# Kernel optimization log

Hardware: AMD Instinct MI355X
Metric: run time of the kernel (lower is better)

## Reference

```python
import jax, jax.numpy as jnp
import numpy as np

B, T, D, H = 16, 1024, 2048, 512


def _lstm_dir(x, w_ih, w_hh, b_ih, b_hh, reverse):
    # x: (B,T,Din); w_ih: (4H,Din); w_hh: (4H,H). PyTorch gate order: i,f,g,o.
    h_dim = w_hh.shape[1]
    xg = jnp.einsum('btd,gd->btg', x, w_ih) + b_ih + b_hh  # (B,T,4H) input gates precomputed

    def step(carry, xg_t):
        h, c = carry
        g = xg_t + h @ w_hh.T
        i, f, gg, o = jnp.split(g, 4, axis=-1)
        i = jax.nn.sigmoid(i)
        f = jax.nn.sigmoid(f)
        gg = jnp.tanh(gg)
        o = jax.nn.sigmoid(o)
        c = f * c + i * gg
        h = o * jnp.tanh(c)
        return (h, c), h

    b = x.shape[0]
    init = (jnp.zeros((b, h_dim), x.dtype), jnp.zeros((b, h_dim), x.dtype))
    _, hs = jax.lax.scan(step, init, jnp.swapaxes(xg, 0, 1), reverse=reverse)
    return jnp.swapaxes(hs, 0, 1)  # (B,T,H)


def _bilstm_layer(x, p_fwd, p_bwd):
    out_f = _lstm_dir(x, *p_fwd, reverse=False)
    out_b = _lstm_dir(x, *p_bwd, reverse=True)
    return jnp.concatenate([out_f, out_b], axis=-1)  # (B,T,2H)


def setup_inputs() -> dict:
    key = jax.random.key(0)
    ks = jax.random.split(key, 20)
    s = 1.0 / np.sqrt(H)

    def u(k, shape):
        return jax.random.uniform(k, shape, jnp.float32, -s, s)

    inp = {'x': jax.random.normal(ks[0], (B, T, D), jnp.float32)}
    i = 1
    for layer, din in [(0, D), (1, 2 * H)]:
        for suf in ['', '_rev']:
            inp[f'w_ih_l{layer}{suf}'] = u(ks[i], (4 * H, din)); i += 1
            inp[f'w_hh_l{layer}{suf}'] = u(ks[i], (4 * H, H)); i += 1
            inp[f'b_ih_l{layer}{suf}'] = u(ks[i], (4 * H,)); i += 1
            inp[f'b_hh_l{layer}{suf}'] = u(ks[i], (4 * H,)); i += 1
            i -= 2  # reuse keys sparingly
            inp[f'b_ih_l{layer}{suf}'] = u(jax.random.fold_in(ks[i], 1), (4 * H,))
            inp[f'b_hh_l{layer}{suf}'] = u(jax.random.fold_in(ks[i], 2), (4 * H,))
            i += 2
    inp['attn_w'] = u(ks[17], (1, 2 * H))
    inp['attn_b'] = u(ks[18], (1,))
    return inp


def reference(x,
              w_ih_l0, w_hh_l0, b_ih_l0, b_hh_l0,
              w_ih_l0_rev, w_hh_l0_rev, b_ih_l0_rev, b_hh_l0_rev,
              w_ih_l1, w_hh_l1, b_ih_l1, b_hh_l1,
              w_ih_l1_rev, w_hh_l1_rev, b_ih_l1_rev, b_hh_l1_rev,
              attn_w, attn_b):
    out = _bilstm_layer(x,
                        (w_ih_l0, w_hh_l0, b_ih_l0, b_hh_l0),
                        (w_ih_l0_rev, w_hh_l0_rev, b_ih_l0_rev, b_hh_l0_rev))
    out = _bilstm_layer(out,
                        (w_ih_l1, w_hh_l1, b_ih_l1, b_hh_l1),
                        (w_ih_l1_rev, w_hh_l1_rev, b_ih_l1_rev, b_hh_l1_rev))
    # attention pooling: Linear(2H -> 1), softmax over time, weighted sum
    scores = jnp.einsum('bth,oh->bto', out, attn_w) + attn_b  # (B,T,1)
    weights = jax.nn.softmax(scores, axis=1)
    encoding = jnp.sum(weights * out, axis=1)  # (B, 2H)
    return encoding
```

## Files before the change

kernel.cpp:

```cpp
#include <hip/hip_runtime.h>
#include <hip/hip_bf16.h>
#include <cstdio>

typedef unsigned short ushort_t;
typedef unsigned long long u64;
typedef __attribute__((ext_vector_type(4))) float f32x4;
typedef __attribute__((ext_vector_type(4))) unsigned int u32x4;
typedef __attribute__((ext_vector_type(8))) __bf16 bf16x8;
typedef __attribute__((ext_vector_type(8))) unsigned short u16x8;
typedef __attribute__((ext_vector_type(4))) unsigned short u16x4;

#define B_  16
#define T_  1024
#define H_  512
#define NG  2048
#define M_  (B_*T_)
#define NBLK_DIR 16
#define FLG_STRIDE 64

__device__ inline unsigned short f2bf_rne(float f){
  union { float f; unsigned int u; } v; v.f = f;
  unsigned int u = v.u;
  unsigned int r = (u + 0x7fffu + ((u >> 16) & 1u)) >> 16;
  return (unsigned short)r;
}
__device__ inline float bf2f(unsigned short s){
  union { unsigned int u; float f; } v; v.u = ((unsigned int)s) << 16;
  return v.f;
}
__device__ inline float sigm_f(float x){
  return 1.0f / (1.0f + __expf(-x));
}
__device__ inline float tanh_f(float x){
  return 1.0f - 2.0f / (__expf(2.0f * x) + 1.0f);
}

__global__ void zero_u32(unsigned* __restrict__ p, int n){
  int i = blockIdx.x * blockDim.x + threadIdx.x;
  if (i < n) p[i] = 0u;
}

__global__ void split_f32_bf16(const float* __restrict__ src,
                               ushort_t* __restrict__ hi, ushort_t* __restrict__ lo,
                               int n4){
  int i = blockIdx.x * blockDim.x + threadIdx.x;
  int stride = gridDim.x * blockDim.x;
  for (; i < n4; i += stride){
    f32x4 v = ((const f32x4*)src)[i];
    u16x4 h4, l4;
    #pragma unroll
    for (int j = 0; j < 4; j++){
      unsigned short h = f2bf_rne(v[j]);
      h4[j] = h;
      l4[j] = f2bf_rne(v[j] - bf2f(h));
    }
    ((u16x4*)hi)[i] = h4;
    ((u16x4*)lo)[i] = l4;
  }
}

__global__ __launch_bounds__(256) void gemm_xg(
    const ushort_t* __restrict__ Ahi, const ushort_t* __restrict__ Alo,
    const ushort_t* __restrict__ Bhi0, const ushort_t* __restrict__ Blo0,
    const ushort_t* __restrict__ Bhi1, const ushort_t* __restrict__ Blo1,
    const float* __restrict__ bi0, const float* __restrict__ bh0,
    const float* __restrict__ bi1, const float* __restrict__ bh1,
    float* __restrict__ C0, float* __restrict__ C1,
    int M, int N, int K)
{
  __shared__ ushort_t As[128*32];
  __shared__ ushort_t Bs[128*32];
  const int tid  = threadIdx.x;
  const int wave = tid >> 6, lane = tid & 63;
  const int l15 = lane & 15, l4 = lane >> 4;
  const int wr = wave >> 1, wc = wave & 1;
  const int n0 = blockIdx.x * 128, m0 = blockIdx.y * 128;
  const int dir = blockIdx.z;
  const ushort_t* Bhi = dir ? Bhi1 : Bhi0;
  const ushort_t* Blo = dir ? Blo1 : Blo0;
  const float* bia = dir ? bi1 : bi0;
  const float* bib = dir ? bh1 : bh0;
  float* C = dir ? C1 : C0;

  f32x4 acc[4][4];
  #pragma unroll
  for (int i = 0; i < 4; i++)
    #pragma unroll
    for (int j = 0; j < 4; j++) acc[i][j] = (f32x4){0.f,0.f,0.f,0.f};

  const int e0 = tid, e1 = 256 + tid;
  const int row0 = e0 >> 2, c80 = (e0 & 3) * 8;
  const int row1 = e1 >> 2, c81 = (e1 & 3) * 8;

  for (int seg = 0; seg < 3; ++seg){
    const ushort_t* Ap = (seg == 2) ? Alo : Ahi;
    const ushort_t* Bp = (seg == 1) ? Blo : Bhi;
    for (int kt = 0; kt < K; kt += 32){
      __builtin_amdgcn_global_load_lds(
        (const __attribute__((address_space(1))) unsigned int*)(Ap + (size_t)(m0 + row0) * K + kt + c80),
        (__attribute__((address_space(3))) unsigned int*)(As + e0 * 8), 16, 0, 0);
      __builtin_amdgcn_global_load_lds(
        (const __attribute__((address_space(1))) unsigned int*)(Bp + (size_t)(n0 + row0) * K + kt + c80),
        (__attribute__((address_space(3))) unsigned int*)(Bs + e0 * 8), 16, 0, 0);
      __builtin_amdgcn_global_load_lds(
        (const __attribute__((address_space(1))) unsigned int*)(Ap + (size_t)(m0 + row1) * K + kt + c81),
        (__attribute__((address_space(3))) unsigned int*)(As + e1 * 8), 16, 0, 0);
      __builtin_amdgcn_global_load_lds(
        (const __attribute__((address_space(1))) unsigned int*)(Bp + (size_t)(n0 + row1) * K + kt + c81),
        (__attribute__((address_space(3))) unsigned int*)(Bs + e1 * 8), 16, 0, 0);
      __syncthreads();
      bf16x8 af[4], bfr[4];
      #pragma unroll
      for (int m = 0; m < 4; m++)
        af[m] = *(const bf16x8*)(As + (wr*64 + m*16 + l15) * 32 + l4 * 8);
      #pragma unroll
      for (int n = 0; n < 4; n++)
        bfr[n] = *(const bf16x8*)(Bs + (wc*64 + n*16 + l15) * 32 + l4 * 8);
      #pragma unroll
      for (int m = 0; m < 4; m++)
        #pragma unroll
        for (int n = 0; n < 4; n++)
          acc[m][n] = __builtin_amdgcn_mfma_f32_16x16x32_bf16(af[m], bfr[n], acc[m][n], 0, 0, 0);
      __syncthreads();
    }
  }
  #pragma unroll
  for (int m = 0; m < 4; m++)
    #pragma unroll
    for (int n = 0; n < 4; n++){
      int col = n0 + wc*64 + n*16 + l15;
      float bias = bia[col] + bib[col];
      #pragma unroll
      for (int r = 0; r < 4; r++){
        int row = m0 + wr*64 + m*16 + l4*4 + r;
        C[(size_t)row * N + col] = acc[m][n][r] + bias;
      }
    }
}

__global__ __launch_bounds__(512, 1) void lstm_layer(
    const float* __restrict__ whh_fwd, const float* __restrict__ whh_bwd,
    const float* __restrict__ xg,
    u64* __restrict__ hbuf,
    unsigned* __restrict__ flags,
    float* __restrict__ out_f32,
    ushort_t* __restrict__ out_hi,
    ushort_t* __restrict__ out_lo)
{
  const int dir = blockIdx.x >> 4;
  const int cb  = blockIdx.x & 15;
  const int tid = threadIdx.x;
  const int wave = tid >> 6, lane = tid & 63;
  const int gate = wave >> 1, ch = wave & 1;
  const int l15 = lane & 15, l4 = lane >> 4;
  const float* whh = dir ? whh_bwd : whh_fwd;
  u64* hb = hbuf + (size_t)dir * 2 * 8192;
  unsigned* flg = flags + (size_t)dir * FLG_STRIDE;

  __shared__ ushort_t hfhi[8192];
  __shared__ ushort_t hflo[8192];
  __shared__ float gbuf[4][16][33];

  bf16x8 Whi[16], Wlo[16];
  {
    const int wrow = gate * 512 + cb * 32 + ch * 16 + l15;
    const float* p0 = whh + (size_t)wrow * 512;
    #pragma unroll
    for (int s = 0; s < 16; s++){
      const float* p = p0 + s * 32 + l4 * 8;
      f32x4 va = *(const f32x4*)(p);
      f32x4 vb = *(const f32x4*)(p + 4);
      u16x8 th, tl;
      #pragma unroll
      for (int j = 0; j < 4; j++){
        unsigned short h = f2bf_rne(va[j]);
        th[j] = h; tl[j] = f2bf_rne(va[j] - bf2f(h));
        unsigned short h2 = f2bf_rne(vb[j]);
        th[4+j] = h2; tl[4+j] = f2bf_rne(vb[j] - bf2f(h2));
      }
      Whi[s] = __builtin_bit_cast(bf16x8, th);
      Wlo[s] = __builtin_bit_cast(bf16x8, tl);
    }
  }

  const int eb = tid >> 5, ecl = tid & 31, ecol = cb * 32 + ecl;

  const int srow = (tid >> 2) & 15;
  const int tq = tid >> 6;
  const int sbase = srow * 512 + (tq >> 2) * 32 + (tq & 3) * 8 + (tid & 3) * 2;

  __hip_atomic_store(&hb[eb * 512 + ecol], (u64)1u << 32, __ATOMIC_RELAXED, __HIP_MEMORY_SCOPE_AGENT);
  if (tid == 0)
    __hip_atomic_store(&flg[cb], 1u, __ATOMIC_RELAXED, __HIP_MEMORY_SCOPE_AGENT);

  float c_state = 0.0f;

  for (int t = 0; t < T_; ++t){
    const int t_eff = dir ? (T_ - 1 - t) : t;
    const float* xgp = xg + ((size_t)dir * M_ + (size_t)eb * T_ + t_eff) * NG + ecol;
    float xi = xgp[0];
    float xf = xgp[512];
    float xgg = xgp[1024];
    float xo = xgp[1536];

    const unsigned want = (unsigned)(t + 1);
    if (tid < NBLK_DIR){
      while (__hip_atomic_load(&flg[tid], __ATOMIC_RELAXED, __HIP_MEMORY_SCOPE_AGENT) < want)
        __builtin_amdgcn_s_sleep(1);
    }
    __syncthreads();

    const u64* src = hb + (size_t)(t & 1) * 8192;
    u64 va[8], vb[8];
    #pragma unroll
    for (int i = 0; i < 8; i++){
      va[i] = __hip_atomic_load(&src[sbase + i * 64],     __ATOMIC_RELAXED, __HIP_MEMORY_SCOPE_AGENT);
      vb[i] = __hip_atomic_load(&src[sbase + i * 64 + 1], __ATOMIC_RELAXED, __HIP_MEMORY_SCOPE_AGENT);
    }
    for (;;){
      unsigned stale = 0;
      #pragma unroll
      for (int i = 0; i < 8; i++){
        if ((unsigned)(va[i] >> 32) != want || (unsigned)(vb[i] >> 32) != want)
          stale |= 1u << i;
      }
      if (!stale) break;
      #pragma unroll
      for (int i = 0; i < 8; i++){
        if (stale & (1u << i)){
          va[i] = __hip_atomic_load(&src[sbase + i * 64],     __ATOMIC_RELAXED, __HIP_MEMORY_SCOPE_AGENT);
          vb[i] = __hip_atomic_load(&src[sbase + i * 64 + 1], __ATOMIC_RELAXED, __HIP_MEMORY_SCOPE_AGENT);
        }
      }
    }
    #pragma unroll
    for (int i = 0; i < 8; i++){
      unsigned d0 = (unsigned)va[i], d1 = (unsigned)vb[i];
      ((unsigned*)hfhi)[i * 512 + tid] = (d0 & 0xffffu) | (d1 << 16);
      ((unsigned*)hflo)[i * 512 + tid] = (d0 >> 16) | (d1 & 0xffff0000u);
    }
    __syncthreads();

    {
      f32x4 a0 = {0.f,0.f,0.f,0.f}, a1 = a0, a2 = a0;
      #pragma unroll
      for (int s = 0; s < 16; s++){
        bf16x8 ah = *(const bf16x8*)&hfhi[(s * 64 + l4 * 16 + l15) * 8];
        bf16x8 al = *(const bf16x8*)&hflo[(s * 64 + l4 * 16 + l15) * 8];
        a0 = __builtin_amdgcn_mfma_f32_16x16x32_bf16(ah, Whi[s], a0, 0, 0, 0);
        a1 = __builtin_amdgcn_mfma_f32_16x16x32_bf16(ah, Wlo[s], a1, 0, 0, 0);
        a2 = __builtin_amdgcn_mfma_f32_16x16x32_bf16(al, Whi[s], a2, 0, 0, 0);
      }
      f32x4 acc = a0 + a1;
      acc = acc + a2;
      #pragma unroll
      for (int r = 0; r < 4; r++)
        gbuf[gate][l4 * 4 + r][ch * 16 + l15] = acc[r];
    }
    __syncthreads();

    {
      float pi = gbuf[0][eb][ecl] + xi;
      float pf = gbuf[1][eb][ecl] + xf;
      float pg = gbuf[2][eb][ecl] + xgg;
      float po = gbuf[3][eb][ecl] + xo;
      float ig = sigm_f(pi);
      float fg = sigm_f(pf);
      float gg = tanh_f(pg);
      float og = sigm_f(po);
      c_state = fg * c_state + ig * gg;
      float h = og * tanh_f(c_state);
      unsigned short hh = f2bf_rne(h);
      unsigned short hl = f2bf_rne(h - bf2f(hh));
      unsigned pack = (unsigned)hh | ((unsigned)hl << 16);
      u64 v = ((u64)(unsigned)(t + 2) << 32) | (u64)pack;
      __hip_atomic_store(&hb[(size_t)((t + 1) & 1) * 8192 + eb * 512 + ecol], v,
                         __ATOMIC_RELAXED, __HIP_MEMORY_SCOPE_AGENT);
      if (tid == 0)
        __hip_atomic_store(&flg[cb], (unsigned)(t + 2), __ATOMIC_RELAXED, __HIP_MEMORY_SCOPE_AGENT);
      size_t oidx = ((size_t)eb * T_ + t_eff) * 1024 + dir * 512 + ecol;
      if (out_f32) out_f32[oidx] = h;
      if (out_hi){ out_hi[oidx] = hh; out_lo[oidx] = hl; }
    }
  }
}

__device__ inline float dot4(f32x4 a, f32x4 b){
  return a[0]*b[0] + a[1]*b[1] + a[2]*b[2] + a[3]*b[3];
}

__global__ __launch_bounds__(256) void attn_pool(
    const float* __restrict__ out1,
    const float* __restrict__ aw,
    const float* __restrict__ ab,
    float* __restrict__ enc)
{
  __shared__ float wbuf[1024];
  __shared__ float sc[1024];
  __shared__ float red[16];
  const int b = blockIdx.x;
  const int tid = threadIdx.x;
  const int wave = tid >> 6, lane = tid & 63;
  ((f32x4*)wbuf)[tid] = ((const f32x4*)aw)[tid];
  __syncthreads();
  const float* ob = out1 + (size_t)b * T_ * 1024;
  const float bias = ab[0];

  for (int t = wave; t < T_; t += 4){
    const float* row = ob + (size_t)t * 1024;
    float s = dot4(((const f32x4*)row)[lane],       ((const f32x4*)wbuf)[lane])
            + dot4(((const f32x4*)row)[lane + 64],  ((const f32x4*)wbuf)[lane + 64])
            + dot4(((const f32x4*)row)[lane + 128], ((const f32x4*)wbuf)[lane + 128])
            + dot4(((const f32x4*)row)[lane + 192], ((const f32x4*)wbuf)[lane + 192]);
    #pragma unroll
    for (int o = 32; o > 0; o >>= 1) s += __shfl_xor(s, o, 64);
    if (lane == 0) sc[t] = s + bias;
  }
  __syncthreads();

  float m = -1e30f;
  for (int i = tid; i < 1024; i += 256) m = fmaxf(m, sc[i]);
  #pragma unroll
  for (int o = 32; o > 0; o >>= 1) m = fmaxf(m, __shfl_xor(m, o, 64));
  if (lane == 0) red[wave] = m;
  __syncthreads();
  m = fmaxf(fmaxf(red[0], red[1]), fmaxf(red[2], red[3]));

  float ssum = 0.f;
  for (int i = tid; i < 1024; i += 256){
    float p = __expf(sc[i] - m);
    sc[i] = p;
    ssum += p;
  }
  #pragma unroll
  for (int o = 32; o > 0; o >>= 1) ssum += __shfl_xor(ssum, o, 64);
  if (lane == 0) red[8 + wave] = ssum;
  __syncthreads();
  float inv = 1.0f / (red[8] + red[9] + red[10] + red[11]);

  f32x4 a = {0.f,0.f,0.f,0.f};
  for (int t = 0; t < T_; t++){
    f32x4 v = *(const f32x4*)(ob + (size_t)t * 1024 + tid * 4);
    float p = sc[t];
    a[0] += p * v[0]; a[1] += p * v[1]; a[2] += p * v[2]; a[3] += p * v[3];
  }
  f32x4 r = { a[0]*inv, a[1]*inv, a[2]*inv, a[3]*inv };
  *(f32x4*)(enc + (size_t)b * 1024 + tid * 4) = r;
}

extern "C" void kernel_launch(void* const* d_in, const int* in_sizes, int n_in,
                              void* d_out, int out_size, void* d_ws, size_t ws_size,
                              hipStream_t stream)
{
  const float* x        = (const float*)d_in[0];
  const float* w_ih_l0  = (const float*)d_in[1];
  const float* w_hh_l0  = (const float*)d_in[2];
  const float* b_ih_l0  = (const float*)d_in[3];
  const float* b_hh_l0  = (const float*)d_in[4];
  const float* w_ih_l0r = (const float*)d_in[5];
  const float* w_hh_l0r = (const float*)d_in[6];
  const float* b_ih_l0r = (const float*)d_in[7];
  const float* b_hh_l0r = (const float*)d_in[8];
  const float* w_ih_l1  = (const float*)d_in[9];
  const float* w_hh_l1  = (const float*)d_in[10];
  const float* b_ih_l1  = (const float*)d_in[11];
  const float* b_hh_l1  = (const float*)d_in[12];
  const float* w_ih_l1r = (const float*)d_in[13];
  const float* w_hh_l1r = (const float*)d_in[14];
  const float* b_ih_l1r = (const float*)d_in[15];
  const float* b_hh_l1r = (const float*)d_in[16];
  const float* attn_w   = (const float*)d_in[17];
  const float* attn_b   = (const float*)d_in[18];
  float* enc = (float*)d_out;

  char* ws = (char*)d_ws;
  size_t off = 0;
  auto alloc = [&](size_t bytes) -> void* {
    void* p = ws + off;
    off += (bytes + 255) & ~(size_t)255;
    return p;
  };
  ushort_t* Ahi  = (ushort_t*)alloc((size_t)M_ * 2048 * 2);
  ushort_t* Alo  = (ushort_t*)alloc((size_t)M_ * 2048 * 2);
  ushort_t* Whi0 = (ushort_t*)alloc((size_t)2048 * 2048 * 2);
  ushort_t* Wlo0 = (ushort_t*)alloc((size_t)2048 * 2048 * 2);
  ushort_t* Whi1 = (ushort_t*)alloc((size_t)2048 * 2048 * 2);
  ushort_t* Wlo1 = (ushort_t*)alloc((size_t)2048 * 2048 * 2);
  float*    xg   = (float*)alloc((size_t)2 * M_ * NG * 4);
  float*    outb = (float*)alloc((size_t)M_ * 1024 * 4);
  u64*      hbuf = (u64*)alloc((size_t)2 * 2 * 2 * 8192 * 8);
  unsigned* flags= (unsigned*)alloc((size_t)2 * 2 * FLG_STRIDE * 4);
  if (off > ws_size){
    fprintf(stderr, "kernel_launch: workspace too small: need %zu have %zu\n", off, ws_size);
    return;
  }

  {
    int n = (int)((size_t)2 * 2 * 2 * 8192 * 8 / 4) + 2 * 2 * FLG_STRIDE;
    zero_u32<<<(n + 255) / 256, 256, 0, stream>>>((unsigned*)hbuf, n);
  }

  split_f32_bf16<<<2048, 256, 0, stream>>>(x, Ahi, Alo, M_ * 2048 / 4);
  split_f32_bf16<<<512, 256, 0, stream>>>(w_ih_l0,  Whi0, Wlo0, 2048 * 2048 / 4);
  split_f32_bf16<<<512, 256, 0, stream>>>(w_ih_l0r, Whi1, Wlo1, 2048 * 2048 / 4);
  gemm_xg<<<dim3(16, 128, 2), 256, 0, stream>>>(
      Ahi, Alo, Whi0, Wlo0, Whi1, Wlo1,
      b_ih_l0, b_hh_l0, b_ih_l0r, b_hh_l0r,
      xg, xg + (size_t)M_ * NG, M_, NG, 2048);
  lstm_layer<<<32, 512, 0, stream>>>(w_hh_l0, w_hh_l0r, xg, hbuf, flags,
                                     nullptr, Ahi, Alo);
  split_f32_bf16<<<512, 256, 0, stream>>>(w_ih_l1,  Whi0, Wlo0, 2048 * 1024 / 4);
  split_f32_bf16<<<512, 256, 0, stream>>>(w_ih_l1r, Whi1, Wlo1, 2048 * 1024 / 4);
  gemm_xg<<<dim3(16, 128, 2), 256, 0, stream>>>(
      Ahi, Alo, Whi0, Wlo0, Whi1, Wlo1,
      b_ih_l1, b_hh_l1, b_ih_l1r, b_hh_l1r,
      xg, xg + (size_t)M_ * NG, M_, NG, 1024);
  lstm_layer<<<32, 512, 0, stream>>>(w_hh_l1, w_hh_l1r, xg,
                                     hbuf + (size_t)2 * 2 * 8192,
                                     flags + (size_t)2 * FLG_STRIDE,
                                     outb, nullptr, nullptr);
  attn_pool<<<16, 256, 0, stream>>>(outb, attn_w, attn_b, enc);
}
```

Before: 10.99 ms.

## Store hidden-state exchange buffer block-contiguous and swizzle LDS staging layout

The global hidden-state exchange buffer is reindexed so each block writes its 512 values contiguously (cb*512+tid) instead of scattered by batch row. Readers then fetch from contiguous per-producer chunks. The LDS staging of the hi/lo bf16 operands is also rewritten with an XOR swizzle to avoid bank conflicts on the MFMA operand reads. The goal is better coalescing of the per-step cross-block polling loads and stores on the recurrent critical path, at the cost of more complex index math.

```diff
diff --git a/kernel.cpp b/kernel.cpp
--- a/kernel.cpp
+++ b/kernel.cpp
@@ -185,11 +185,15 @@
 
   const int eb = tid >> 5, ecl = tid & 31, ecol = cb * 32 + ecl;
 
-  const int srow = (tid >> 2) & 15;
-  const int tq = tid >> 6;
-  const int sbase = srow * 512 + (tq >> 2) * 32 + (tq & 3) * 8 + (tid & 3) * 2;
-
-  __hip_atomic_store(&hb[eb * 512 + ecol], (u64)1u << 32, __ATOMIC_RELAXED, __HIP_MEMORY_SCOPE_AGENT);
+  const int p  = tid >> 5;
+  const int a  = tid & 15;
+  const int rh = (tid >> 4) & 1;
+  const int qh = p * 4 + (a >> 2);
+  const int jp = a & 3;
+  const int swz = qh & 7;
+  const size_t cbase = (size_t)p * 512 + rh * 256 + 2 * a;
+
+  __hip_atomic_store(&hb[cb * 512 + tid], (u64)1u << 32, __ATOMIC_RELAXED, __HIP_MEMORY_SCOPE_AGENT);
   if (tid == 0)
     __hip_atomic_store(&flg[cb], 1u, __ATOMIC_RELAXED, __HIP_MEMORY_SCOPE_AGENT);
 
@@ -210,12 +214,12 @@
     }
     __syncthreads();
 
-    const u64* src = hb + (size_t)(t & 1) * 8192;
+    const u64* src = hb + (size_t)(t & 1) * 8192 + cbase;
     u64 va[8], vb[8];
     #pragma unroll
     for (int i = 0; i < 8; i++){
-      va[i] = __hip_atomic_load(&src[sbase + i * 64],     __ATOMIC_RELAXED, __HIP_MEMORY_SCOPE_AGENT);
-      vb[i] = __hip_atomic_load(&src[sbase + i * 64 + 1], __ATOMIC_RELAXED, __HIP_MEMORY_SCOPE_AGENT);
+      va[i] = __hip_atomic_load(&src[i * 32],     __ATOMIC_RELAXED, __HIP_MEMORY_SCOPE_AGENT);
+      vb[i] = __hip_atomic_load(&src[i * 32 + 1], __ATOMIC_RELAXED, __HIP_MEMORY_SCOPE_AGENT);
     }
     for (;;){
       unsigned stale = 0;
@@ -228,16 +232,20 @@
       #pragma unroll
       for (int i = 0; i < 8; i++){
         if (stale & (1u << i)){
-          va[i] = __hip_atomic_load(&src[sbase + i * 64],     __ATOMIC_RELAXED, __HIP_MEMORY_SCOPE_AGENT);
-          vb[i] = __hip_atomic_load(&src[sbase + i * 64 + 1], __ATOMIC_RELAXED, __HIP_MEMORY_SCOPE_AGENT);
+          va[i] = __hip_atomic_load(&src[i * 32],     __ATOMIC_RELAXED, __HIP_MEMORY_SCOPE_AGENT);
+          vb[i] = __hip_atomic_load(&src[i * 32 + 1], __ATOMIC_RELAXED, __HIP_MEMORY_SCOPE_AGENT);
         }
       }
     }
     #pragma unroll
     for (int i = 0; i < 8; i++){
       unsigned d0 = (unsigned)va[i], d1 = (unsigned)vb[i];
-      ((unsigned*)hfhi)[i * 512 + tid] = (d0 & 0xffffu) | (d1 << 16);
-      ((unsigned*)hflo)[i * 512 + tid] = (d0 >> 16) | (d1 & 0xffff0000u);
+      unsigned hi = (d0 & 0xffffu) | (d1 << 16);
+      unsigned lo = (d0 >> 16) | (d1 & 0xffff0000u);
+      int row = rh * 8 + i;
+      int qp = qh * 16 + (row ^ swz);
+      ((unsigned*)hfhi)[qp * 4 + jp] = hi;
+      ((unsigned*)hflo)[qp * 4 + jp] = lo;
     }
     __syncthreads();
 
@@ -245,8 +253,10 @@
       f32x4 a0 = {0.f,0.f,0.f,0.f}, a1 = a0, a2 = a0;
       #pragma unroll
       for (int s = 0; s < 16; s++){
-        bf16x8 ah = *(const bf16x8*)&hfhi[(s * 64 + l4 * 16 + l15) * 8];
-        bf16x8 al = *(const bf16x8*)&hflo[(s * 64 + l4 * 16 + l15) * 8];
+        int qhr = s * 4 + l4;
+        int qpr = qhr * 16 + (l15 ^ (qhr & 7));
+        bf16x8 ah = *(const bf16x8*)&hfhi[qpr * 8];
+        bf16x8 al = *(const bf16x8*)&hflo[qpr * 8];
         a0 = __builtin_amdgcn_mfma_f32_16x16x32_bf16(ah, Whi[s], a0, 0, 0, 0);
         a1 = __builtin_amdgcn_mfma_f32_16x16x32_bf16(ah, Wlo[s], a1, 0, 0, 0);
         a2 = __builtin_amdgcn_mfma_f32_16x16x32_bf16(al, Whi[s], a2, 0, 0, 0);
@@ -274,7 +284,7 @@
       unsigned short hl = f2bf_rne(h - bf2f(hh));
       unsigned pack = (unsigned)hh | ((unsigned)hl << 16);
       u64 v = ((u64)(unsigned)(t + 2) << 32) | (u64)pack;
-      __hip_atomic_store(&hb[(size_t)((t + 1) & 1) * 8192 + eb * 512 + ecol], v,
+      __hip_atomic_store(&hb[(size_t)((t + 1) & 1) * 8192 + cb * 512 + tid], v,
                          __ATOMIC_RELAXED, __HIP_MEMORY_SCOPE_AGENT);
       if (tid == 0)
         __hip_atomic_store(&flg[cb], (unsigned)(t + 2), __ATOMIC_RELAXED, __HIP_MEMORY_SCOPE_AGENT);
```

Result: faster. 10.12 ms (-7.9%).
